# Performance work log

Measured on AMD Instinct MI355X. Metric: run time of the kernel, lower is better.

The kernel has to match this reference:

```python
import jax, jax.numpy as jnp
import numpy as np

T = 4096
HIDDEN = 2048
N_HEADS = 16
N_KV_HEADS = 4
HEAD_DIM = 128
WINDOW = 1024  # per_layer_sliding_window = WINDOW + 1 -> q attends keys with q_pos - k_pos <= WINDOW
ROPE_THETA = 100000.0
QKV_OUT = (N_HEADS + 2 * N_KV_HEADS) * HEAD_DIM  # 3072


def setup_inputs() -> dict:
    key = jax.random.key(0)
    k1, k2, k3, k4 = jax.random.split(key, 4)
    return {
        "hidden_states": jax.random.normal(k1, (T, HIDDEN), dtype=jnp.float32),
        "positions": jnp.arange(T, dtype=jnp.int32),
        "w_qkv": jax.random.normal(k2, (HIDDEN, QKV_OUT), dtype=jnp.float32) * 0.02,
        "b_qkv": jax.random.normal(k3, (QKV_OUT,), dtype=jnp.float32) * 0.02,
        "w_o": jax.random.normal(k4, (N_HEADS * HEAD_DIM, HIDDEN), dtype=jnp.float32) * 0.02,
    }


def _apply_rope(x, positions):
    # x: [T, n_heads, HEAD_DIM], neox-style rotary over full head dim
    half = HEAD_DIM // 2
    inv_freq = 1.0 / (ROPE_THETA ** (jnp.arange(half, dtype=jnp.float32) / half))
    freqs = positions.astype(jnp.float32)[:, None] * inv_freq[None, :]  # [T, half]
    cos = jnp.cos(freqs)[:, None, :]  # [T, 1, half]
    sin = jnp.sin(freqs)[:, None, :]
    x1, x2 = x[..., :half], x[..., half:]
    return jnp.concatenate([x1 * cos - x2 * sin, x2 * cos + x1 * sin], axis=-1)


def reference(hidden_states, positions, w_qkv, b_qkv, w_o):
    # QKV projection (bias=True)
    qkv = hidden_states @ w_qkv + b_qkv  # [T, QKV_OUT]
    q_size = N_HEADS * HEAD_DIM
    kv_size = N_KV_HEADS * HEAD_DIM
    q = qkv[:, :q_size].reshape(T, N_HEADS, HEAD_DIM)
    k = qkv[:, q_size:q_size + kv_size].reshape(T, N_KV_HEADS, HEAD_DIM)
    v = qkv[:, q_size + kv_size:].reshape(T, N_KV_HEADS, HEAD_DIM)

    # RoPE on q and k
    q = _apply_rope(q, positions)
    k = _apply_rope(k, positions)

    # GQA: expand kv heads to match query heads
    group = N_HEADS // N_KV_HEADS
    k = jnp.repeat(k, group, axis=1)  # [T, N_HEADS, HEAD_DIM]
    v = jnp.repeat(v, group, axis=1)

    scale = HEAD_DIM ** -0.5
    scores = jnp.einsum('qhd,khd->hqk', q, k) * scale  # [H, T, T]

    # causal + sliding-window mask: j <= i and i - j <= WINDOW
    i = jnp.arange(T)[:, None]
    j = jnp.arange(T)[None, :]
    mask = (j <= i) & (i - j <= WINDOW)  # [T, T]
    scores = jnp.where(mask[None, :, :], scores, jnp.finfo(scores.dtype).min)

    probs = jax.nn.softmax(scores, axis=-1)
    attn = jnp.einsum('hqk,khd->qhd', probs, v)  # [T, H, HEAD_DIM]
    attn = attn.reshape(T, N_HEADS * HEAD_DIM)

    # output projection (bias=False)
    return attn @ w_o
```

## Files before the change

### kernel.cpp

```cpp
#include <hip/hip_runtime.h>
#include <cstdint>

#define T_TOK 4096
#define HID 2048
#define NH 16
#define NKV 4
#define HD 128
#define WIN 1024
#define QKVO 3072

typedef float f32x4 __attribute__((ext_vector_type(4)));
typedef float f32x16 __attribute__((ext_vector_type(16)));
typedef __bf16 bf16x8 __attribute__((ext_vector_type(8)));
typedef __bf16 bf16x4 __attribute__((ext_vector_type(4)));
typedef unsigned int u32x4 __attribute__((ext_vector_type(4)));

__device__ __forceinline__ void gload16(const void* g, void* lds) {
  auto gp = reinterpret_cast<__attribute__((address_space(1))) void*>(
      reinterpret_cast<uintptr_t>(g));
  auto lp = reinterpret_cast<__attribute__((address_space(3))) void*>(
      reinterpret_cast<uintptr_t>(lds));
  __builtin_amdgcn_global_load_lds(gp, lp, 16, 0, 0);
}

__device__ __forceinline__ f32x4 mfma16(bf16x8 a, bf16x8 b, f32x4 c) {
  return __builtin_amdgcn_mfma_f32_16x16x32_bf16(a, b, c, 0, 0, 0);
}
__device__ __forceinline__ f32x16 mfma32(bf16x8 a, bf16x8 b, f32x16 c) {
  return __builtin_amdgcn_mfma_f32_32x32x16_bf16(a, b, c, 0, 0, 0);
}
__device__ __forceinline__ unsigned cvtpk(float lo, float hi) {
  unsigned r;
  asm("v_cvt_pk_bf16_f32 %0, %1, %2" : "=v"(r) : "v"(lo), "v"(hi));
  return r;
}
__device__ __forceinline__ void pl32swap(unsigned& a, unsigned& b) {
  asm volatile("v_permlane32_swap_b32 %0, %1" : "+v"(a), "+v"(b));
}

__global__ __launch_bounds__(256) void k_f32_to_bf16(const float* __restrict__ x,
                                                     __bf16* __restrict__ y) {
  const size_t e = (size_t)blockIdx.x * 256 + threadIdx.x;
  const float4* xv = (const float4*)x;
  float4 a = xv[e * 2], b = xv[e * 2 + 1];
  bf16x8 o;
  o[0] = (__bf16)a.x; o[1] = (__bf16)a.y; o[2] = (__bf16)a.z; o[3] = (__bf16)a.w;
  o[4] = (__bf16)b.x; o[5] = (__bf16)b.y; o[6] = (__bf16)b.z; o[7] = (__bf16)b.w;
  *(bf16x8*)(y + e * 8) = o;
}

__global__ __launch_bounds__(256) void k_transpose2(
    const float* __restrict__ W1, __bf16* __restrict__ Wt1,
    const float* __restrict__ W2, __bf16* __restrict__ Wt2) {
  __shared__ float lt[64][69];
  int bid = blockIdx.x;
  const float* W;
  __bf16* Wt;
  int R, C;
  if (bid < 1536) {
    W = W1; Wt = Wt1; R = HID; C = QKVO;
  } else {
    bid -= 1536; W = W2; Wt = Wt2; R = HID; C = HID;
  }
  const int nbx = C >> 6;
  const int c0 = (bid % nbx) << 6;
  const int r0 = (bid / nbx) << 6;
  const int tid = threadIdx.x;
  const int tx = tid & 15, ty = tid >> 4;
#pragma unroll
  for (int i = 0; i < 4; i++) {
    const int r = ty + 16 * i;
    const float4 v = *(const float4*)(W + (size_t)(r0 + r) * C + c0 + 4 * tx);
    lt[r][4 * tx] = v.x;
    lt[r][4 * tx + 1] = v.y;
    lt[r][4 * tx + 2] = v.z;
    lt[r][4 * tx + 3] = v.w;
  }
  __syncthreads();
  const int ux = tid & 7, uy = tid >> 3;
#pragma unroll
  for (int i = 0; i < 2; i++) {
    const int c = uy + 32 * i;
    bf16x8 o;
#pragma unroll
    for (int k = 0; k < 8; k++) o[k] = (__bf16)lt[8 * ux + k][c];
    *(bf16x8*)(Wt + (size_t)(c0 + c) * R + r0 + 8 * ux) = o;
  }
}

__global__ void k_rope_tab(const int* __restrict__ pos, float* __restrict__ cosT,
                           float* __restrict__ sinT) {
  const int t = blockIdx.x;
  const int d = threadIdx.x;
  const float inv = exp2f(-(float)d * (16.609640474436812f / 64.0f));
  const float fr = (float)pos[t] * inv;
  cosT[t * 64 + d] = cosf(fr);
  sinT[t * 64 + d] = sinf(fr);
}

template <bool BIAS, typename OutT>
__global__ __launch_bounds__(256, 2) void k_gemm(const __bf16* __restrict__ A,
                                                 const __bf16* __restrict__ Bt,
                                                 const float* __restrict__ bias,
                                                 OutT* __restrict__ C,
                                                 int M, int N, int K) {
  __shared__ __align__(16) __bf16 As[2][128 * 64];
  __shared__ __align__(16) __bf16 Bs[2][128 * 64];
  const int tid = threadIdx.x;
  const int lane = tid & 63;
  const int w = tid >> 6;
  const int wr = w >> 1, wc = w & 1;
  const int c = lane & 15, g = lane >> 4;
  const int csw = (c & 7) << 4;

  const int nstc = N >> 9;
  const int bid = blockIdx.x;
  const int xcd = bid & 7;
  const int j = bid >> 3;
  const int spx = (int)(gridDim.x >> 7);
  const int s = xcd * spx + (j >> 4);
  const int q = j & 15;
  const int by = (s / nstc) * 4 + (q >> 2);
  const int bx = (s % nstc) * 4 + (q & 3);
  const int m0 = by << 7, n0 = bx << 7;

  const int o0 = w * 4096 + lane * 16;
  const int srow = 32 * w + (lane >> 3);
  const int schunk = (lane & 7) ^ ((lane >> 3) & 7);
  const __bf16* gA0 = A + (size_t)(m0 + srow) * K + schunk * 8;
  const __bf16* gB0 = Bt + (size_t)(n0 + srow) * K + schunk * 8;

  f32x4 acc[4][4] = {};

  {
    char* la = (char*)&As[0][0];
    char* lb = (char*)&Bs[0][0];
#pragma unroll
    for (int qq = 0; qq < 4; qq++) {
      gload16(gA0 + (size_t)qq * 8 * K, la + o0 + qq * 1024);
      gload16(gB0 + (size_t)qq * 8 * K, lb + o0 + qq * 1024);
    }
  }
  __syncthreads();

  int cur = 0;
  for (int kt = 0; kt < K; kt += 64) {
    if (kt + 64 < K) {
      char* la = (char*)&As[0][0] + (cur ^ 1) * 16384;
      char* lb = (char*)&Bs[0][0] + (cur ^ 1) * 16384;
#pragma unroll
      for (int qq = 0; qq < 4; qq++) {
        gload16(gA0 + kt + 64 + (size_t)qq * 8 * K, la + o0 + qq * 1024);
        gload16(gB0 + kt + 64 + (size_t)qq * 8 * K, lb + o0 + qq * 1024);
      }
    }
    const char* as = (const char*)&As[0][0] + cur * 16384;
    const char* bs = (const char*)&Bs[0][0] + cur * 16384;
#pragma unroll
    for (int ds = 0; ds < 2; ds++) {
      bf16x8 af[4], bfr[4];
#pragma unroll
      for (int mi = 0; mi < 4; mi++)
        af[mi] = *(const bf16x8*)(as + (wr * 64 + mi * 16 + c) * 128 +
                                  ((ds * 64 + g * 16) ^ csw));
#pragma unroll
      for (int ni = 0; ni < 4; ni++)
        bfr[ni] = *(const bf16x8*)(bs + (wc * 64 + ni * 16 + c) * 128 +
                                   ((ds * 64 + g * 16) ^ csw));
#pragma unroll
      for (int mi = 0; mi < 4; mi++)
#pragma unroll
        for (int ni = 0; ni < 4; ni++)
          acc[mi][ni] = mfma16(af[mi], bfr[ni], acc[mi][ni]);
    }
    __syncthreads();
    cur ^= 1;
  }

#pragma unroll
  for (int ni = 0; ni < 4; ni++) {
    const int col = n0 + wc * 64 + ni * 16 + c;
    const float bv = BIAS ? bias[col] : 0.0f;
#pragma unroll
    for (int mi = 0; mi < 4; mi++)
#pragma unroll
      for (int r = 0; r < 4; r++) {
        const int row = m0 + wr * 64 + mi * 16 + 4 * g + r;
        C[(size_t)row * N + col] = (OutT)(acc[mi][ni][r] + bv);
      }
  }
}

__global__ __launch_bounds__(256) void k_rope_pack(
    const __bf16* __restrict__ qkv, const float* __restrict__ cosT,
    const float* __restrict__ sinT, __bf16* __restrict__ Qp,
    __bf16* __restrict__ Kp, __bf16* __restrict__ Vf) {
  const int t0 = blockIdx.x * 64;
  const int hh = blockIdx.y;
  const int tid = threadIdx.x;
  const int col0 = hh * HD;
  __shared__ __bf16 lt[64][136];
  if (hh < NH + NKV) {
    const bool isq = hh < NH;
    const float s = isq ? (0.08838834764831845f * 1.4426950408889634f) : 1.0f;
    __bf16* base = isq ? (Qp + (size_t)hh * T_TOK * HD)
                       : (Kp + (size_t)(hh - NH) * T_TOK * HD);
#pragma unroll
    for (int jj = 0; jj < 2; jj++) {
      const int e = jj * 256 + tid;
      const int tl = e >> 3, ch = e & 7;
      const int tt = t0 + tl;
      const bf16x8 x1 = *(const bf16x8*)(qkv + (size_t)tt * QKVO + col0 + ch * 8);
      const bf16x8 x2 = *(const bf16x8*)(qkv + (size_t)tt * QKVO + col0 + 64 + ch * 8);
      const float4 c0 = *(const float4*)(cosT + tt * 64 + ch * 8);
      const float4 c1 = *(const float4*)(cosT + tt * 64 + ch * 8 + 4);
      const float4 s0 = *(const float4*)(sinT + tt * 64 + ch * 8);
      const float4 s1 = *(const float4*)(sinT + tt * 64 + ch * 8 + 4);
      const float cs[8] = {c0.x, c0.y, c0.z, c0.w, c1.x, c1.y, c1.z, c1.w};
      const float sn[8] = {s0.x, s0.y, s0.z, s0.w, s1.x, s1.y, s1.z, s1.w};
      bf16x8 o1, o2;
#pragma unroll
      for (int i = 0; i < 8; i++) {
        const float a = (float)x1[i], b = (float)x2[i];
        o1[i] = (__bf16)((a * cs[i] - b * sn[i]) * s);
        o2[i] = (__bf16)((b * cs[i] + a * sn[i]) * s);
      }
      const int d2s = isq ? ch * 8 : ((ch * 8) ^ ((tt & 7) << 3));
      __bf16* dst = base + (size_t)tt * HD;
      *(bf16x8*)(dst + d2s) = o1;
      *(bf16x8*)(dst + 64 + d2s) = o2;
    }
  } else {
    const int kv = hh - (NH + NKV);
#pragma unroll
    for (int jj = 0; jj < 4; jj++) {
      const int e = jj * 256 + tid;
      const int tl = e >> 4, dc = e & 15;
      *(bf16x8*)&lt[tl][dc * 8] =
          *(const bf16x8*)(qkv + (size_t)(t0 + tl) * QKVO + col0 + dc * 8);
    }
    __syncthreads();
    __bf16* outb = Vf + ((size_t)kv * 64 + (t0 >> 6)) * 8192;
#pragma unroll
    for (int jj = 0; jj < 4; jj++) {
      const int u = jj * 256 + tid;
      const int lu = u & 63, ks = (u >> 6) & 3, m = u >> 8;
      const int d = m * 32 + (lu & 31);
      const int tb = ks * 16 + ((lu >> 5) << 3);
      bf16x8 o;
#pragma unroll
      for (int j = 0; j < 8; j++) o[j] = lt[tb + j][d];
      *(bf16x8*)(outb + (size_t)u * 8) = o;
    }
  }
}

__global__ __launch_bounds__(256, 2) void k_attn(const __bf16* __restrict__ Qp,
                                                 const __bf16* __restrict__ Kp,
                                                 const __bf16* __restrict__ Vf,
                                                 __bf16* __restrict__ attnO) {
  __shared__ __align__(16) __bf16 Ks[2][64 * 128];

  const int tid = threadIdx.x;
  const int lane = tid & 63;
  const int w = tid >> 6;
  const int l31 = lane & 31;
  const int hi = lane >> 5;
  const int swz = (lane & 7) << 4;
  const int bid = blockIdx.x;
  const int xcd = bid & 7, j = bid >> 3;
  const int h = ((xcd >> 1) << 2) + ((xcd & 1) << 1) + (j & 1);
  const int qb = 31 - (j >> 1);
  const int kvh = h >> 2;
  const int q0 = qb * 128;
  const int iw = q0 + 32 * w;
  const int irow = iw + l31;

  bf16x8 qf[8];
  {
    const __bf16* qbase = Qp + ((size_t)h * T_TOK + irow) * HD;
#pragma unroll
    for (int ds = 0; ds < 8; ds++)
      qf[ds] = *(const bf16x8*)(qbase + ds * 16 + hi * 8);
  }

  f32x16 ot[4] = {};
  float mrun = 0.0f, lrun = 0.0f;

  const int jstart = (q0 >= WIN) ? (q0 - WIN) : 0;
  const int niter = (q0 + 128 - jstart) >> 6;

  const char* Kg = (const char*)Kp + (size_t)kvh * T_TOK * HD * 2;
  const char* kg0 = Kg + (size_t)(jstart + 16 * w + (lane >> 4)) * 256 + (lane & 15) * 16;
  const __bf16* Vgb = Vf + (size_t)kvh * 64 * 8192;

#pragma unroll
  for (int q = 0; q < 4; q++)
    gload16(kg0 + q * 1024, (char*)&Ks[0][0] + w * 4096 + q * 1024);

  int cur = 0;

  for (int it = 0; it < niter; ++it) {
    const int j0 = jstart + it * 64;
    __syncthreads();

    if (it + 1 < niter) {
      const char* kg = kg0 + (size_t)(it + 1) * 16384;
      char* kd = (char*)&Ks[cur ^ 1][0] + w * 4096;
#pragma unroll
      for (int q = 0; q < 4; q++) gload16(kg + q * 1024, kd + q * 1024);
    }

    if (j0 > iw + 31) { cur ^= 1; continue; }
    if (iw - (j0 + 63) > WIN) { cur ^= 1; continue; }

    const __bf16* vt = Vgb + (size_t)(j0 >> 6) * 8192;
    bf16x8 vf[4][4];
#pragma unroll
    for (int m = 0; m < 4; m++)
#pragma unroll
      for (int ks = 0; ks < 4; ks++)
        vf[m][ks] = *(const bf16x8*)(vt + (m * 256 + ks * 64 + lane) * 8);

    const char* kb = (const char*)&Ks[cur][0];

    f32x16 st[2] = {};
    __builtin_amdgcn_s_setprio(1);
#pragma unroll
    for (int t = 0; t < 2; t++)
#pragma unroll
      for (int ds = 0; ds < 8; ds++) {
        bf16x8 kf = *(const bf16x8*)(kb + (t * 32 + l31) * 256 +
                                     ((ds * 32 + hi * 16) ^ swz));
        st[t] = mfma32(kf, qf[ds], st[t]);
      }
    __builtin_amdgcn_s_setprio(0);

    float p[2][16];
    float cmax = -1e30f;
    const bool interior = (j0 + 63 <= iw) && (iw + 31 - j0 <= WIN);
    if (interior) {
#pragma unroll
      for (int t = 0; t < 2; t++)
#pragma unroll
        for (int r = 0; r < 16; r++) {
          const float s = st[t][r];
          p[t][r] = s;
          cmax = fmaxf(cmax, s);
        }
    } else {
      const int jb = irow - j0 - 4 * hi;
#pragma unroll
      for (int t = 0; t < 2; t++)
#pragma unroll
        for (int r = 0; r < 16; r++) {
          float s = st[t][r];
          const int off = 32 * t + (r & 3) + 8 * (r >> 2);
          s = ((unsigned)(jb - off) <= WIN) ? s : -1e30f;
          p[t][r] = s;
          cmax = fmaxf(cmax, s);
        }
    }
    cmax = fmaxf(cmax, __shfl_xor(cmax, 32));

    if (!__all(cmax <= mrun + 11.54f)) {
      const float mn = fmaxf(mrun, cmax);
      const float alpha = exp2f(mrun - mn);
      lrun *= alpha;
#pragma unroll
      for (int m = 0; m < 4; m++) ot[m] *= alpha;
      mrun = mn;
    }
    float rs = 0.0f;
#pragma unroll
    for (int t = 0; t < 2; t++)
#pragma unroll
      for (int r = 0; r < 16; r++) {
        const float e_ = exp2f(p[t][r] - mrun);
        p[t][r] = e_;
        rs += e_;
      }
    rs += __shfl_xor(rs, 32);
    lrun += rs;

    bf16x8 pb[4];
#pragma unroll
    for (int t = 0; t < 2; t++) {
      unsigned wds[8];
#pragma unroll
      for (int i = 0; i < 8; i++) wds[i] = cvtpk(p[t][2 * i], p[t][2 * i + 1]);
      pl32swap(wds[0], wds[2]);
      pl32swap(wds[1], wds[3]);
      pl32swap(wds[4], wds[6]);
      pl32swap(wds[5], wds[7]);
      u32x4 f0 = {wds[0], wds[1], wds[2], wds[3]};
      u32x4 f1 = {wds[4], wds[5], wds[6], wds[7]};
      pb[2 * t] = __builtin_bit_cast(bf16x8, f0);
      pb[2 * t + 1] = __builtin_bit_cast(bf16x8, f1);
    }

    __builtin_amdgcn_s_setprio(1);
#pragma unroll
    for (int m = 0; m < 4; m++)
#pragma unroll
      for (int ks = 0; ks < 4; ks++)
        ot[m] = mfma32(vf[m][ks], pb[ks], ot[m]);
    __builtin_amdgcn_s_setprio(0);

    cur ^= 1;
  }

  const float inv_l = 1.0f / lrun;
  __bf16* orow = attnO + (size_t)irow * (NH * HD) + h * HD;
#pragma unroll
  for (int m = 0; m < 4; m++)
#pragma unroll
    for (int rg = 0; rg < 4; rg++) {
      const int d0 = 32 * m + 8 * rg + 4 * hi;
      bf16x4 o4;
#pragma unroll
      for (int r = 0; r < 4; r++) o4[r] = (__bf16)(ot[m][4 * rg + r] * inv_l);
      *(bf16x4*)(orow + d0) = o4;
    }
}

extern "C" void kernel_launch(void* const* d_in, const int* in_sizes, int n_in,
                              void* d_out, int out_size, void* d_ws, size_t ws_size,
                              hipStream_t stream) {
  (void)in_sizes; (void)n_in; (void)out_size; (void)ws_size;
  const float* hidden = (const float*)d_in[0];
  const int* positions = (const int*)d_in[1];
  const float* w_qkv = (const float*)d_in[2];
  const float* b_qkv = (const float*)d_in[3];
  const float* w_o = (const float*)d_in[4];
  float* out = (float*)d_out;

  char* ws = (char*)d_ws;
  __bf16* Hb = (__bf16*)ws;    ws += (size_t)T_TOK * HID * 2;
  __bf16* Wqkvt = (__bf16*)ws; ws += (size_t)QKVO * HID * 2;
  __bf16* Wot = (__bf16*)ws;   ws += (size_t)HID * HID * 2;
  float* cosT = (float*)ws;    ws += (size_t)T_TOK * 64 * 4;
  float* sinT = (float*)ws;    ws += (size_t)T_TOK * 64 * 4;
  __bf16* qkv = (__bf16*)ws;   ws += (size_t)T_TOK * QKVO * 2;
  __bf16* Qp = (__bf16*)ws;    ws += (size_t)NH * T_TOK * HD * 2;
  __bf16* Kp = (__bf16*)ws;    ws += (size_t)NKV * T_TOK * HD * 2;
  __bf16* Vfb = (__bf16*)ws;   ws += (size_t)NKV * 64 * 8192 * 2;
  __bf16* attnb = (__bf16*)ws; ws += (size_t)T_TOK * NH * HD * 2;

  k_f32_to_bf16<<<T_TOK * HID / (256 * 8), 256, 0, stream>>>(hidden, Hb);
  k_transpose2<<<2560, 256, 0, stream>>>(w_qkv, Wqkvt, w_o, Wot);
  k_rope_tab<<<T_TOK, 64, 0, stream>>>(positions, cosT, sinT);
  k_gemm<true, __bf16><<<(T_TOK / 128) * (QKVO / 128), 256, 0, stream>>>(
      Hb, Wqkvt, b_qkv, qkv, T_TOK, QKVO, HID);
  k_rope_pack<<<dim3(T_TOK / 64, NH + 2 * NKV), 256, 0, stream>>>(
      qkv, cosT, sinT, Qp, Kp, Vfb);
  k_attn<<<512, 256, 0, stream>>>(Qp, Kp, Vfb, attnb);
  k_gemm<false, float><<<(T_TOK / 128) * (HID / 128), 256, 0, stream>>>(
      attnb, Wot, nullptr, out, T_TOK, HID, HID);
}
```

Before: 178.5 us.

## Fuse RoPE and QKV packing into GEMM epilogue; software-pipeline QK in attention

The QKV GEMM epilogue now stages each 128x128 tile in LDS and applies RoPE, scaling and the Q/K/V packed layouts directly. This removes the intermediate qkv buffer and the separate rope_pack kernel. The attention loop is restructured so the QK^T MFMAs for the next K tile run before the current PV MFMAs, with a two-ahead K prefetch, to overlap softmax with matrix work. The cost is more register pressure and an extra LDS round-trip inside the GEMM epilogue.

```diff
diff --git a/kernel.cpp b/kernel.cpp
--- a/kernel.cpp
+++ b/kernel.cpp
@@ -98,14 +98,14 @@
   sinT[t * 64 + d] = sinf(fr);
 }
 
-template <bool BIAS, typename OutT>
-__global__ __launch_bounds__(256, 2) void k_gemm(const __bf16* __restrict__ A,
-                                                 const __bf16* __restrict__ Bt,
-                                                 const float* __restrict__ bias,
-                                                 OutT* __restrict__ C,
-                                                 int M, int N, int K) {
-  __shared__ __align__(16) __bf16 As[2][128 * 64];
-  __shared__ __align__(16) __bf16 Bs[2][128 * 64];
+template <int MODE>
+__global__ __launch_bounds__(256, 2) void k_gemm(
+    const __bf16* __restrict__ A, const __bf16* __restrict__ Bt,
+    const float* __restrict__ bias, float* __restrict__ C,
+    const float* __restrict__ cosT, const float* __restrict__ sinT,
+    __bf16* __restrict__ Qp, __bf16* __restrict__ Kp, __bf16* __restrict__ Vf,
+    int M, int N, int K) {
+  __shared__ __align__(16) __bf16 smem[32768];
   const int tid = threadIdx.x;
   const int lane = tid & 63;
   const int w = tid >> 6;
@@ -133,8 +133,8 @@
   f32x4 acc[4][4] = {};
 
   {
-    char* la = (char*)&As[0][0];
-    char* lb = (char*)&Bs[0][0];
+    char* la = (char*)smem;
+    char* lb = (char*)smem + 32768;
 #pragma unroll
     for (int qq = 0; qq < 4; qq++) {
       gload16(gA0 + (size_t)qq * 8 * K, la + o0 + qq * 1024);
@@ -146,16 +146,16 @@
   int cur = 0;
   for (int kt = 0; kt < K; kt += 64) {
     if (kt + 64 < K) {
-      char* la = (char*)&As[0][0] + (cur ^ 1) * 16384;
-      char* lb = (char*)&Bs[0][0] + (cur ^ 1) * 16384;
+      char* la = (char*)smem + (cur ^ 1) * 16384;
+      char* lb = (char*)smem + 32768 + (cur ^ 1) * 16384;
 #pragma unroll
       for (int qq = 0; qq < 4; qq++) {
         gload16(gA0 + kt + 64 + (size_t)qq * 8 * K, la + o0 + qq * 1024);
         gload16(gB0 + kt + 64 + (size_t)qq * 8 * K, lb + o0 + qq * 1024);
       }
     }
-    const char* as = (const char*)&As[0][0] + cur * 16384;
-    const char* bs = (const char*)&Bs[0][0] + cur * 16384;
+    const char* as = (const char*)smem + cur * 16384;
+    const char* bs = (const char*)smem + 32768 + cur * 16384;
 #pragma unroll
     for (int ds = 0; ds < 2; ds++) {
       bf16x8 af[4], bfr[4];
@@ -177,80 +177,80 @@
     cur ^= 1;
   }
 
-#pragma unroll
-  for (int ni = 0; ni < 4; ni++) {
-    const int col = n0 + wc * 64 + ni * 16 + c;
-    const float bv = BIAS ? bias[col] : 0.0f;
-#pragma unroll
-    for (int mi = 0; mi < 4; mi++)
-#pragma unroll
-      for (int r = 0; r < 4; r++) {
-        const int row = m0 + wr * 64 + mi * 16 + 4 * g + r;
-        C[(size_t)row * N + col] = (OutT)(acc[mi][ni][r] + bv);
-      }
-  }
-}
-
-__global__ __launch_bounds__(256) void k_rope_pack(
-    const __bf16* __restrict__ qkv, const float* __restrict__ cosT,
-    const float* __restrict__ sinT, __bf16* __restrict__ Qp,
-    __bf16* __restrict__ Kp, __bf16* __restrict__ Vf) {
-  const int t0 = blockIdx.x * 64;
-  const int hh = blockIdx.y;
-  const int tid = threadIdx.x;
-  const int col0 = hh * HD;
-  __shared__ __bf16 lt[64][136];
-  if (hh < NH + NKV) {
-    const bool isq = hh < NH;
-    const float s = isq ? (0.08838834764831845f * 1.4426950408889634f) : 1.0f;
-    __bf16* base = isq ? (Qp + (size_t)hh * T_TOK * HD)
-                       : (Kp + (size_t)(hh - NH) * T_TOK * HD);
-#pragma unroll
-    for (int jj = 0; jj < 2; jj++) {
-      const int e = jj * 256 + tid;
-      const int tl = e >> 3, ch = e & 7;
-      const int tt = t0 + tl;
-      const bf16x8 x1 = *(const bf16x8*)(qkv + (size_t)tt * QKVO + col0 + ch * 8);
-      const bf16x8 x2 = *(const bf16x8*)(qkv + (size_t)tt * QKVO + col0 + 64 + ch * 8);
-      const float4 c0 = *(const float4*)(cosT + tt * 64 + ch * 8);
-      const float4 c1 = *(const float4*)(cosT + tt * 64 + ch * 8 + 4);
-      const float4 s0 = *(const float4*)(sinT + tt * 64 + ch * 8);
-      const float4 s1 = *(const float4*)(sinT + tt * 64 + ch * 8 + 4);
-      const float cs[8] = {c0.x, c0.y, c0.z, c0.w, c1.x, c1.y, c1.z, c1.w};
-      const float sn[8] = {s0.x, s0.y, s0.z, s0.w, s1.x, s1.y, s1.z, s1.w};
-      bf16x8 o1, o2;
-#pragma unroll
-      for (int i = 0; i < 8; i++) {
-        const float a = (float)x1[i], b = (float)x2[i];
-        o1[i] = (__bf16)((a * cs[i] - b * sn[i]) * s);
-        o2[i] = (__bf16)((b * cs[i] + a * sn[i]) * s);
-      }
-      const int d2s = isq ? ch * 8 : ((ch * 8) ^ ((tt & 7) << 3));
-      __bf16* dst = base + (size_t)tt * HD;
-      *(bf16x8*)(dst + d2s) = o1;
-      *(bf16x8*)(dst + 64 + d2s) = o2;
+  if constexpr (MODE == 0) {
+#pragma unroll
+    for (int ni = 0; ni < 4; ni++) {
+      const int col = n0 + wc * 64 + ni * 16 + c;
+#pragma unroll
+      for (int mi = 0; mi < 4; mi++)
+#pragma unroll
+        for (int r = 0; r < 4; r++) {
+          const int row = m0 + wr * 64 + mi * 16 + 4 * g + r;
+          C[(size_t)row * N + col] = acc[mi][ni][r];
+        }
     }
   } else {
-    const int kv = hh - (NH + NKV);
-#pragma unroll
-    for (int jj = 0; jj < 4; jj++) {
-      const int e = jj * 256 + tid;
-      const int tl = e >> 4, dc = e & 15;
-      *(bf16x8*)&lt[tl][dc * 8] =
-          *(const bf16x8*)(qkv + (size_t)(t0 + tl) * QKVO + col0 + dc * 8);
+    __bf16* sm = smem;
+#pragma unroll
+    for (int ni = 0; ni < 4; ni++) {
+      const int col = wc * 64 + ni * 16 + c;
+      const float bv = bias[n0 + col];
+#pragma unroll
+      for (int mi = 0; mi < 4; mi++)
+#pragma unroll
+        for (int r = 0; r < 4; r++)
+          sm[(wr * 64 + mi * 16 + 4 * g + r) * 136 + col] =
+              (__bf16)(acc[mi][ni][r] + bv);
     }
     __syncthreads();
-    __bf16* outb = Vf + ((size_t)kv * 64 + (t0 >> 6)) * 8192;
-#pragma unroll
-    for (int jj = 0; jj < 4; jj++) {
-      const int u = jj * 256 + tid;
-      const int lu = u & 63, ks = (u >> 6) & 3, m = u >> 8;
-      const int d = m * 32 + (lu & 31);
-      const int tb = ks * 16 + ((lu >> 5) << 3);
-      bf16x8 o;
-#pragma unroll
-      for (int j = 0; j < 8; j++) o[j] = lt[tb + j][d];
-      *(bf16x8*)(outb + (size_t)u * 8) = o;
+
+    if (n0 < (NH + NKV) * HD) {
+      const bool isq = n0 < NH * HD;
+      const float sc = isq ? (0.08838834764831845f * 1.4426950408889634f) : 1.0f;
+      __bf16* base = isq ? (Qp + (size_t)(n0 >> 7) * T_TOK * HD)
+                         : (Kp + (size_t)((n0 >> 7) - NH) * T_TOK * HD);
+#pragma unroll
+      for (int jj = 0; jj < 4; jj++) {
+        const int e = jj * 256 + tid;
+        const int tl = e >> 3, ch = e & 7;
+        const int tt = m0 + tl;
+        const bf16x8 x1 = *(const bf16x8*)(sm + tl * 136 + ch * 8);
+        const bf16x8 x2 = *(const bf16x8*)(sm + tl * 136 + 64 + ch * 8);
+        const float4 c0 = *(const float4*)(cosT + tt * 64 + ch * 8);
+        const float4 c1 = *(const float4*)(cosT + tt * 64 + ch * 8 + 4);
+        const float4 s0 = *(const float4*)(sinT + tt * 64 + ch * 8);
+        const float4 s1 = *(const float4*)(sinT + tt * 64 + ch * 8 + 4);
+        const float cs[8] = {c0.x, c0.y, c0.z, c0.w, c1.x, c1.y, c1.z, c1.w};
+        const float sn[8] = {s0.x, s0.y, s0.z, s0.w, s1.x, s1.y, s1.z, s1.w};
+        bf16x8 o1, o2;
+#pragma unroll
+        for (int i = 0; i < 8; i++) {
+          const float a = (float)x1[i], b = (float)x2[i];
+          o1[i] = (__bf16)((a * cs[i] - b * sn[i]) * sc);
+          o2[i] = (__bf16)((b * cs[i] + a * sn[i]) * sc);
+        }
+        const int d2s = isq ? ch * 8 : ((ch * 8) ^ ((tt & 7) << 3));
+        __bf16* dst = base + (size_t)tt * HD;
+        *(bf16x8*)(dst + d2s) = o1;
+        *(bf16x8*)(dst + 64 + d2s) = o2;
+      }
+    } else {
+      const int kv = (n0 >> 7) - (NH + NKV);
+#pragma unroll
+      for (int st2 = 0; st2 < 2; st2++) {
+        __bf16* outb = Vf + ((size_t)kv * 64 + (m0 >> 6) + st2) * 8192;
+#pragma unroll
+        for (int jj = 0; jj < 4; jj++) {
+          const int u = jj * 256 + tid;
+          const int lu = u & 63, ks = (u >> 6) & 3, mq = u >> 8;
+          const int d = mq * 32 + (lu & 31);
+          const int tb = st2 * 64 + ks * 16 + ((lu >> 5) << 3);
+          bf16x8 o;
+#pragma unroll
+          for (int jz = 0; jz < 8; jz++) o[jz] = sm[(tb + jz) * 136 + d];
+          *(bf16x8*)(outb + (size_t)u * 8) = o;
+        }
+      }
     }
   }
 }
@@ -268,9 +268,9 @@
   const int hi = lane >> 5;
   const int swz = (lane & 7) << 4;
   const int bid = blockIdx.x;
-  const int xcd = bid & 7, j = bid >> 3;
-  const int h = ((xcd >> 1) << 2) + ((xcd & 1) << 1) + (j & 1);
-  const int qb = 31 - (j >> 1);
+  const int xcd = bid & 7, jj = bid >> 3;
+  const int h = ((xcd >> 1) << 2) + ((xcd & 1) << 1) + (jj & 1);
+  const int qb = 31 - (jj >> 1);
   const int kvh = h >> 2;
   const int q0 = qb * 128;
   const int iw = q0 + 32 * w;
@@ -294,120 +294,135 @@
   const char* kg0 = Kg + (size_t)(jstart + 16 * w + (lane >> 4)) * 256 + (lane & 15) * 16;
   const __bf16* Vgb = Vf + (size_t)kvh * 64 * 8192;
 
-#pragma unroll
-  for (int q = 0; q < 4; q++)
-    gload16(kg0 + q * 1024, (char*)&Ks[0][0] + w * 4096 + q * 1024);
-
-  int cur = 0;
-
-  for (int it = 0; it < niter; ++it) {
-    const int j0 = jstart + it * 64;
+  auto STAGE = [&](int t, int bufi) {
+    const char* kg = kg0 + (size_t)t * 16384;
+    char* kd = (char*)&Ks[bufi][0] + w * 4096;
+#pragma unroll
+    for (int q = 0; q < 4; q++) gload16(kg + q * 1024, kd + q * 1024);
+  };
+
+  f32x16 st[2];
+  auto QK = [&](int bufi) {
+    const char* kb = (const char*)&Ks[bufi][0];
+    f32x16 z = {};
+    st[0] = z;
+    st[1] = z;
+    __builtin_amdgcn_s_setprio(1);
+#pragma unroll
+    for (int t2 = 0; t2 < 2; t2++)
+#pragma unroll
+      for (int ds = 0; ds < 8; ds++) {
+        bf16x8 kf = *(const bf16x8*)(kb + (t2 * 32 + l31) * 256 +
+                                     ((ds * 32 + hi * 16) ^ swz));
+        st[t2] = mfma32(kf, qf[ds], st[t2]);
+      }
+    __builtin_amdgcn_s_setprio(0);
+  };
+
+  STAGE(0, 0);
+  __syncthreads();
+  if (niter > 1) STAGE(1, 1);
+  {
+    const int j0 = jstart;
+    if (!((j0 > iw + 31) || (iw - (j0 + 63) > WIN))) QK(0);
+  }
+
+  for (int t = 0; t < niter; ++t) {
+    const int j0 = jstart + t * 64;
+    const bool act = !((j0 > iw + 31) || (iw - (j0 + 63) > WIN));
+
+    bf16x8 vf[4][4];
+    bf16x8 pb[4];
+    if (act) {
+      const __bf16* vt = Vgb + (size_t)(j0 >> 6) * 8192;
+#pragma unroll
+      for (int m = 0; m < 4; m++)
+#pragma unroll
+        for (int ks = 0; ks < 4; ks++)
+          vf[m][ks] = *(const bf16x8*)(vt + (m * 256 + ks * 64 + lane) * 8);
+
+      float p[2][16];
+      float cmax = -1e30f;
+      const bool interior = (j0 + 63 <= iw) && (iw + 31 - j0 <= WIN);
+      if (interior) {
+#pragma unroll
+        for (int t2 = 0; t2 < 2; t2++)
+#pragma unroll
+          for (int r = 0; r < 16; r++) {
+            const float s = st[t2][r];
+            p[t2][r] = s;
+            cmax = fmaxf(cmax, s);
+          }
+      } else {
+        const int jb = irow - j0 - 4 * hi;
+#pragma unroll
+        for (int t2 = 0; t2 < 2; t2++)
+#pragma unroll
+          for (int r = 0; r < 16; r++) {
+            float s = st[t2][r];
+            const int off = 32 * t2 + (r & 3) + 8 * (r >> 2);
+            s = ((unsigned)(jb - off) <= WIN) ? s : -1e30f;
+            p[t2][r] = s;
+            cmax = fmaxf(cmax, s);
+          }
+      }
+      cmax = fmaxf(cmax, __shfl_xor(cmax, 32));
+
+      if (!__all(cmax <= mrun + 11.54f)) {
+        const float mn = fmaxf(mrun, cmax);
+        const float alpha = exp2f(mrun - mn);
+        lrun *= alpha;
+#pragma unroll
+        for (int m = 0; m < 4; m++) ot[m] *= alpha;
+        mrun = mn;
+      }
+      float rs = 0.0f;
+#pragma unroll
+      for (int t2 = 0; t2 < 2; t2++)
+#pragma unroll
+        for (int r = 0; r < 16; r++) {
+          const float e_ = exp2f(p[t2][r] - mrun);
+          p[t2][r] = e_;
+          rs += e_;
+        }
+      rs += __shfl_xor(rs, 32);
+      lrun += rs;
+
+#pragma unroll
+      for (int t2 = 0; t2 < 2; t2++) {
+        unsigned wds[8];
+#pragma unroll
+        for (int i = 0; i < 8; i++)
+          wds[i] = cvtpk(p[t2][2 * i], p[t2][2 * i + 1]);
+        pl32swap(wds[0], wds[2]);
+        pl32swap(wds[1], wds[3]);
+        pl32swap(wds[4], wds[6]);
+        pl32swap(wds[5], wds[7]);
+        u32x4 f0 = {wds[0], wds[1], wds[2], wds[3]};
+        u32x4 f1 = {wds[4], wds[5], wds[6], wds[7]};
+        pb[2 * t2] = __builtin_bit_cast(bf16x8, f0);
+        pb[2 * t2 + 1] = __builtin_bit_cast(bf16x8, f1);
+      }
+    }
+
     __syncthreads();
 
-    if (it + 1 < niter) {
-      const char* kg = kg0 + (size_t)(it + 1) * 16384;
-      char* kd = (char*)&Ks[cur ^ 1][0] + w * 4096;
-#pragma unroll
-      for (int q = 0; q < 4; q++) gload16(kg + q * 1024, kd + q * 1024);
-    }
-
-    if (j0 > iw + 31) { cur ^= 1; continue; }
-    if (iw - (j0 + 63) > WIN) { cur ^= 1; continue; }
-
-    const __bf16* vt = Vgb + (size_t)(j0 >> 6) * 8192;
-    bf16x8 vf[4][4];
-#pragma unroll
-    for (int m = 0; m < 4; m++)
-#pragma unroll
-      for (int ks = 0; ks < 4; ks++)
-        vf[m][ks] = *(const bf16x8*)(vt + (m * 256 + ks * 64 + lane) * 8);
-
-    const char* kb = (const char*)&Ks[cur][0];
-
-    f32x16 st[2] = {};
-    __builtin_amdgcn_s_setprio(1);
-#pragma unroll
-    for (int t = 0; t < 2; t++)
-#pragma unroll
-      for (int ds = 0; ds < 8; ds++) {
-        bf16x8 kf = *(const bf16x8*)(kb + (t * 32 + l31) * 256 +
-                                     ((ds * 32 + hi * 16) ^ swz));
-        st[t] = mfma32(kf, qf[ds], st[t]);
-      }
-    __builtin_amdgcn_s_setprio(0);
-
-    float p[2][16];
-    float cmax = -1e30f;
-    const bool interior = (j0 + 63 <= iw) && (iw + 31 - j0 <= WIN);
-    if (interior) {
-#pragma unroll
-      for (int t = 0; t < 2; t++)
-#pragma unroll
-        for (int r = 0; r < 16; r++) {
-          const float s = st[t][r];
-          p[t][r] = s;
-          cmax = fmaxf(cmax, s);
-        }
-    } else {
-      const int jb = irow - j0 - 4 * hi;
-#pragma unroll
-      for (int t = 0; t < 2; t++)
-#pragma unroll
-        for (int r = 0; r < 16; r++) {
-          float s = st[t][r];
-          const int off = 32 * t + (r & 3) + 8 * (r >> 2);
-          s = ((unsigned)(jb - off) <= WIN) ? s : -1e30f;
-          p[t][r] = s;
-          cmax = fmaxf(cmax, s);
-        }
-    }
-    cmax = fmaxf(cmax, __shfl_xor(cmax, 32));
-
-    if (!__all(cmax <= mrun + 11.54f)) {
-      const float mn = fmaxf(mrun, cmax);
-      const float alpha = exp2f(mrun - mn);
-      lrun *= alpha;
-#pragma unroll
-      for (int m = 0; m < 4; m++) ot[m] *= alpha;
-      mrun = mn;
-    }
-    float rs = 0.0f;
-#pragma unroll
-    for (int t = 0; t < 2; t++)
-#pragma unroll
-      for (int r = 0; r < 16; r++) {
-        const float e_ = exp2f(p[t][r] - mrun);
-        p[t][r] = e_;
-        rs += e_;
-      }
-    rs += __shfl_xor(rs, 32);
-    lrun += rs;
-
-    bf16x8 pb[4];
-#pragma unroll
-    for (int t = 0; t < 2; t++) {
-      unsigned wds[8];
-#pragma unroll
-      for (int i = 0; i < 8; i++) wds[i] = cvtpk(p[t][2 * i], p[t][2 * i + 1]);
-      pl32swap(wds[0], wds[2]);
-      pl32swap(wds[1], wds[3]);
-      pl32swap(wds[4], wds[6]);
-      pl32swap(wds[5], wds[7]);
-      u32x4 f0 = {wds[0], wds[1], wds[2], wds[3]};
-      u32x4 f1 = {wds[4], wds[5], wds[6], wds[7]};
-      pb[2 * t] = __builtin_bit_cast(bf16x8, f0);
-      pb[2 * t + 1] = __builtin_bit_cast(bf16x8, f1);
-    }
-
-    __builtin_amdgcn_s_setprio(1);
-#pragma unroll
-    for (int m = 0; m < 4; m++)
-#pragma unroll
-      for (int ks = 0; ks < 4; ks++)
-        ot[m] = mfma32(vf[m][ks], pb[ks], ot[m]);
-    __builtin_amdgcn_s_setprio(0);
-
-    cur ^= 1;
+    if (t + 2 < niter) STAGE(t + 2, t & 1);
+    {
+      const int j1 = j0 + 64;
+      if (t + 1 < niter && !((j1 > iw + 31) || (iw - (j1 + 63) > WIN)))
+        QK((t + 1) & 1);
+    }
+
+    if (act) {
+      __builtin_amdgcn_s_setprio(1);
+#pragma unroll
+      for (int m = 0; m < 4; m++)
+#pragma unroll
+        for (int ks = 0; ks < 4; ks++)
+          ot[m] = mfma32(vf[m][ks], pb[ks], ot[m]);
+      __builtin_amdgcn_s_setprio(0);
+    }
   }
 
   const float inv_l = 1.0f / lrun;
@@ -441,7 +456,6 @@
   __bf16* Wot = (__bf16*)ws;   ws += (size_t)HID * HID * 2;
   float* cosT = (float*)ws;    ws += (size_t)T_TOK * 64 * 4;
   float* sinT = (float*)ws;    ws += (size_t)T_TOK * 64 * 4;
-  __bf16* qkv = (__bf16*)ws;   ws += (size_t)T_TOK * QKVO * 2;
   __bf16* Qp = (__bf16*)ws;    ws += (size_t)NH * T_TOK * HD * 2;
   __bf16* Kp = (__bf16*)ws;    ws += (size_t)NKV * T_TOK * HD * 2;
   __bf16* Vfb = (__bf16*)ws;   ws += (size_t)NKV * 64 * 8192 * 2;
@@ -450,11 +464,10 @@
   k_f32_to_bf16<<<T_TOK * HID / (256 * 8), 256, 0, stream>>>(hidden, Hb);
   k_transpose2<<<2560, 256, 0, stream>>>(w_qkv, Wqkvt, w_o, Wot);
   k_rope_tab<<<T_TOK, 64, 0, stream>>>(positions, cosT, sinT);
-  k_gemm<true, __bf16><<<(T_TOK / 128) * (QKVO / 128), 256, 0, stream>>>(
-      Hb, Wqkvt, b_qkv, qkv, T_TOK, QKVO, HID);
-  k_rope_pack<<<dim3(T_TOK / 64, NH + 2 * NKV), 256, 0, stream>>>(
-      qkv, cosT, sinT, Qp, Kp, Vfb);
+  k_gemm<1><<<(T_TOK / 128) * (QKVO / 128), 256, 0, stream>>>(
+      Hb, Wqkvt, b_qkv, nullptr, cosT, sinT, Qp, Kp, Vfb, T_TOK, QKVO, HID);
   k_attn<<<512, 256, 0, stream>>>(Qp, Kp, Vfb, attnb);
-  k_gemm<false, float><<<(T_TOK / 128) * (HID / 128), 256, 0, stream>>>(
-      attnb, Wot, nullptr, out, T_TOK, HID, HID);
-}
+  k_gemm<0><<<(T_TOK / 128) * (HID / 128), 256, 0, stream>>>(
+      attnb, Wot, nullptr, out, nullptr, nullptr, nullptr, nullptr, nullptr,
+      T_TOK, HID, HID);
+}
```

After: 180.2 us. About the same (+1.0%).
